# Kernel optimization log

Measured on AMD Instinct MI355X. Metric: run time of the kernel, lower is better.

The kernel has to match this reference:

```python
import jax, jax.numpy as jnp
import numpy as np

NUM_HEADS = 16
DK = 64
DV = 64
MASK_FILL = -10000000000.0


def setup_inputs() -> dict:
    key = jax.random.key(0)
    kq, kk, kv, km = jax.random.split(key, 4)
    B, L, D = 2, 2048, NUM_HEADS * DK
    Q = jax.random.normal(kq, (B, L, D), dtype=jnp.float32)
    K = jax.random.normal(kk, (B, L, D), dtype=jnp.float32)
    V = jax.random.normal(kv, (B, L, NUM_HEADS * DV), dtype=jnp.float32)
    mask = jax.random.randint(km, (B, L, L), 0, 2).astype(jnp.bool_)
    return {"Q": Q, "K": K, "V": V, "mask": mask}


def reference(Q, K, V, mask):
    B, Lq, _ = Q.shape
    Lk = K.shape[1]
    # split heads: [B, H, L, d]
    q = Q.reshape(B, Lq, NUM_HEADS, DK).transpose(0, 2, 1, 3)
    k = K.reshape(B, Lk, NUM_HEADS, DK).transpose(0, 2, 1, 3)
    v = V.reshape(B, Lk, NUM_HEADS, DV).transpose(0, 2, 1, 3)
    # scores [B, H, Lq, Lk]; NOTE: original masks BEFORE scaling by 1/sqrt(dk)
    scores = jnp.einsum("bhqd,bhkd->bhqk", q, k)
    scores = jnp.where(mask[:, None, :, :], MASK_FILL, scores)
    scores = scores / jnp.sqrt(jnp.asarray(DK, dtype=scores.dtype))
    attn = jax.nn.softmax(scores, axis=-1)
    out = jnp.einsum("bhqk,bhkd->bhqd", attn, v)  # [B, H, Lq, dv]
    # concat heads back: [B, Lq, H*dv]
    return out.transpose(0, 2, 1, 3).reshape(B, Lq, NUM_HEADS * DV)
```

## Files before the change

kernel.cpp:

```cpp
#include <hip/hip_runtime.h>
#include <hip/hip_bf16.h>

#define NH 16
#define DH 64
#define LL 2048
#define DM 1024
#define SCALE2 0.1803368801111204f
#define M_STATIC 10.0f
#define THR_C 6.0f
#define NT2 (LL / 128)

typedef __attribute__((ext_vector_type(4))) float f32x4;
typedef __attribute__((ext_vector_type(8))) short bf16x8;
typedef __attribute__((ext_vector_type(4))) short bf16x4;

__device__ __forceinline__ unsigned pk2(float lo, float hi) {
    __hip_bfloat162 h = __float22bfloat162_rn(make_float2(lo, hi));
    union { __hip_bfloat162 h; unsigned u; } c; c.h = h; return c.u;
}
__device__ __forceinline__ bf16x8 cvt8(float4 a, float4 b) {
    union { bf16x8 v; unsigned u[4]; } r;
    r.u[0] = pk2(a.x, a.y); r.u[1] = pk2(a.z, a.w);
    r.u[2] = pk2(b.x, b.y); r.u[3] = pk2(b.z, b.w);
    return r.v;
}
__device__ __forceinline__ float exp2_fast(float x) {
    float y;
    asm("v_exp_f32 %0, %1" : "=v"(y) : "v"(x));
    return y;
}

__global__ __launch_bounds__(256) void pack_mask2(const void* __restrict__ mask,
                                                  unsigned* __restrict__ bits)
{
    const int tid = threadIdx.x;
    const int lane = tid & 63;
    const int* mw = (const int*)mask;
    unsigned long long bad = __ballot((unsigned)mw[lane] > 1u);
    const bool is_int = (bad == 0ULL);

    const int wid = blockIdx.x * 256 + tid;
    const int g = wid & 3;
    const int t = (wid >> 2) & 15;
    const int q64 = wid >> 6;
    unsigned m = 0;
    if (is_int) {
        const int* p = (const int*)mask + (size_t)q64 * LL + t * 128 + 4 * g;
        #pragma unroll
        for (int sub = 0; sub < 2; ++sub)
            #pragma unroll
            for (int ki = 0; ki < 4; ++ki) {
                int4 v = *(const int4*)(p + sub * 64 + ki * 16);
                int base = sub * 16 + ki * 4;
                m |= (v.x ? 1u : 0u) << base;
                m |= (v.y ? 1u : 0u) << (base + 1);
                m |= (v.z ? 1u : 0u) << (base + 2);
                m |= (v.w ? 1u : 0u) << (base + 3);
            }
    } else {
        const unsigned char* pb = (const unsigned char*)mask
                                + (size_t)q64 * LL + t * 128 + 4 * g;
        #pragma unroll
        for (int sub = 0; sub < 2; ++sub)
            #pragma unroll
            for (int ki = 0; ki < 4; ++ki) {
                unsigned v = *(const unsigned*)(pb + sub * 64 + ki * 16);
                int base = sub * 16 + ki * 4;
                m |= (v & 1u) << base;
                m |= ((v >> 8) & 1u) << (base + 1);
                m |= ((v >> 16) & 1u) << (base + 2);
                m |= ((v >> 24) & 1u) << (base + 3);
            }
    }
    bits[wid] = m;
}

__global__ __launch_bounds__(256) void prep_k(const float* __restrict__ K,
                                              short* __restrict__ Kb)
{
    const int kt = blockIdx.x, h = blockIdx.y, b = blockIdx.z;
    const int tid = threadIdx.x;
    const int key = tid >> 2;
    const int c8 = (tid & 3) * 2;
    const float* src = K + ((size_t)b * LL + kt * 64 + key) * DM + h * DH + c8 * 8;
    float4 a = *(const float4*)(src);
    float4 bb = *(const float4*)(src + 4);
    float4 c = *(const float4*)(src + 8);
    float4 d = *(const float4*)(src + 12);
    short* dst = Kb + (((size_t)(b * NH + h) * 32 + kt) << 12);
    *(bf16x8*)&dst[key * 64 + ((c8 ^ (key & 7)) << 3)] = cvt8(a, bb);
    *(bf16x8*)&dst[key * 64 + (((c8 + 1) ^ (key & 7)) << 3)] = cvt8(c, d);
}

__global__ __launch_bounds__(256) void prep_v(const float* __restrict__ V,
                                              short* __restrict__ Vb)
{
    const int kt = blockIdx.x, h = blockIdx.y, b = blockIdx.z;
    const int tid = threadIdx.x;
    const int kp = tid & 31;
    const int dv8 = tid >> 5;
    const float* s0 = V + ((size_t)b * LL + kt * 64 + 2 * kp) * DM + h * DH + dv8 * 8;
    float4 a0 = *(const float4*)(s0);
    float4 a1 = *(const float4*)(s0 + 4);
    float4 b0 = *(const float4*)(s0 + DM);
    float4 b1 = *(const float4*)(s0 + DM + 4);
    float av[8] = {a0.x, a0.y, a0.z, a0.w, a1.x, a1.y, a1.z, a1.w};
    float bv[8] = {b0.x, b0.y, b0.z, b0.w, b1.x, b1.y, b1.z, b1.w};
    short* dst = Vb + (((size_t)(b * NH + h) * 32 + kt) << 12);
    #pragma unroll
    for (int j = 0; j < 8; ++j) {
        int dv = dv8 * 8 + j;
        int off = dv * 64 + (((kp >> 1) ^ (dv & 15)) << 2) + 2 * (kp & 1);
        *(unsigned*)&dst[off] = pk2(av[j], bv[j]);
    }
}

__global__ __launch_bounds__(512, 4) void mha_fwd2(
    const float* __restrict__ Q, const short* __restrict__ Kb,
    const short* __restrict__ Vb, const unsigned* __restrict__ mbits,
    float* __restrict__ out)
{
    const int bid = blockIdx.x;
    const int xcd = bid & 7;
    const int j = bid >> 3;
    const int pair = xcd * 4 + (j >> 4);
    const int qblk = j & 15;
    const int h = pair & 15;
    const int b = pair >> 4;

    const int tid = threadIdx.x;
    const int w = tid >> 6;
    const int lane = tid & 63;
    const int lq = lane & 15;
    const int g = lane >> 4;

    const int qbase = qblk * 128 + w * 16;

    __shared__ short Kt[2][2][4096];
    __shared__ short Vt[2][2][4096];

    const short* Ktile0 = Kb + ((size_t)(b * NH + h) << 17);
    const short* Vtile0 = Vb + ((size_t)(b * NH + h) << 17);
    const unsigned* Mp = mbits + ((size_t)b * LL + qbase + lq) * 64 + g;

    unsigned mnext = Mp[0];
    #pragma unroll
    for (int sub = 0; sub < 2; ++sub) {
        __builtin_amdgcn_global_load_lds(
            (const unsigned*)(Ktile0 + sub * 4096 + w * 512 + lane * 8),
            (unsigned*)&Kt[0][sub][w * 512], 16, 0, 0);
        __builtin_amdgcn_global_load_lds(
            (const unsigned*)(Vtile0 + sub * 4096 + w * 512 + lane * 8),
            (unsigned*)&Vt[0][sub][w * 512], 16, 0, 0);
    }

    bf16x8 qf[2];
    {
        const float* qrow = Q + ((size_t)b * LL + qbase + lq) * DM + h * DH;
        #pragma unroll
        for (int half = 0; half < 2; ++half) {
            const float* src = qrow + half * 32 + g * 8;
            float4 a = *(const float4*)(src);
            float4 c = *(const float4*)(src + 4);
            a.x *= SCALE2; a.y *= SCALE2; a.z *= SCALE2; a.w *= SCALE2;
            c.x *= SCALE2; c.y *= SCALE2; c.z *= SCALE2; c.w *= SCALE2;
            qf[half] = cvt8(a, c);
        }
    }

    f32x4 o[4];
    #pragma unroll
    for (int t = 0; t < 4; ++t) o[t] = (f32x4){0.f, 0.f, 0.f, 0.f};
    f32x4 l_acc = (f32x4){0.f, 0.f, 0.f, 0.f};
    float m_run = M_STATIC;
    const bf16x4 ones = {(short)0x3F80, (short)0x3F80, (short)0x3F80, (short)0x3F80};

    asm volatile("s_waitcnt vmcnt(0)" ::: "memory");
    __builtin_amdgcn_s_barrier();

    #pragma unroll 2
    for (int t = 0; t < NT2; ++t) {
        const int cur = t & 1;
        const unsigned mword = mnext;
        if (t + 1 < NT2) {
            mnext = Mp[(t + 1) * 4];
            const short* kb = Ktile0 + (size_t)(t + 1) * 8192;
            const short* vb = Vtile0 + (size_t)(t + 1) * 8192;
            #pragma unroll
            for (int sub = 0; sub < 2; ++sub) {
                __builtin_amdgcn_global_load_lds(
                    (const unsigned*)(kb + sub * 4096 + w * 512 + lane * 8),
                    (unsigned*)&Kt[cur ^ 1][sub][w * 512], 16, 0, 0);
                __builtin_amdgcn_global_load_lds(
                    (const unsigned*)(vb + sub * 4096 + w * 512 + lane * 8),
                    (unsigned*)&Vt[cur ^ 1][sub][w * 512], 16, 0, 0);
            }
            asm volatile("s_waitcnt vmcnt(5)" ::: "memory");
        } else {
            asm volatile("s_waitcnt vmcnt(0)" ::: "memory");
        }
        __builtin_amdgcn_s_barrier();
        __builtin_amdgcn_sched_barrier(0);

        f32x4 s[8];
        __builtin_amdgcn_s_setprio(1);
        #pragma unroll
        for (int sub = 0; sub < 2; ++sub)
            #pragma unroll
            for (int ki = 0; ki < 4; ++ki) {
                const int row = ki * 16 + lq;
                bf16x8 k0 = *(const bf16x8*)
                    &Kt[cur][sub][row * 64 + ((g ^ (lq & 7)) << 3)];
                bf16x8 k1 = *(const bf16x8*)
                    &Kt[cur][sub][row * 64 + (((4 + g) ^ (lq & 7)) << 3)];
                f32x4 acc = (f32x4){0.f, 0.f, 0.f, 0.f};
                acc = __builtin_amdgcn_mfma_f32_16x16x32_bf16(k0, qf[0], acc, 0, 0, 0);
                acc = __builtin_amdgcn_mfma_f32_16x16x32_bf16(k1, qf[1], acc, 0, 0, 0);
                s[sub * 4 + ki] = acc;
            }
        __builtin_amdgcn_s_setprio(0);

        f32x4 sv[8];
        #pragma unroll
        for (int i = 0; i < 8; ++i) sv[i] = s[i] - m_run;

        f32x4 mx = sv[0];
        #pragma unroll
        for (int i = 1; i < 8; ++i) {
            mx[0] = fmaxf(mx[0], sv[i][0]);
            mx[1] = fmaxf(mx[1], sv[i][1]);
            mx[2] = fmaxf(mx[2], sv[i][2]);
            mx[3] = fmaxf(mx[3], sv[i][3]);
        }
        float pmax = fmaxf(fmaxf(mx[0], mx[1]), fmaxf(mx[2], mx[3]));
        if (!__all(pmax <= THR_C)) {
            float tmax = fmaxf(pmax, __shfl_xor(pmax, 16, 64));
            tmax = fmaxf(tmax, __shfl_xor(tmax, 32, 64));
            float shift = fmaxf(tmax, 0.f);
            float alpha = exp2_fast(-shift);
            m_run += shift;
            #pragma unroll
            for (int q = 0; q < 4; ++q) {
                o[q][0] *= alpha; o[q][1] *= alpha;
                o[q][2] *= alpha; o[q][3] *= alpha;
            }
            l_acc[0] *= alpha; l_acc[1] *= alpha;
            l_acc[2] *= alpha; l_acc[3] *= alpha;
            #pragma unroll
            for (int i = 0; i < 8; ++i) sv[i] = sv[i] - shift;
        }

        float p_[32];
        #pragma unroll
        for (int i = 0; i < 8; ++i)
            #pragma unroll
            for (int r = 0; r < 4; ++r)
                p_[i * 4 + r] = exp2_fast(sv[i][r]);

        const unsigned nword = ~mword;
        #pragma unroll
        for (int idx = 0; idx < 32; ++idx) {
            int keep = (int)(nword << (31 - idx)) >> 31;
            unsigned pu = __builtin_bit_cast(unsigned, p_[idx]) & (unsigned)keep;
            p_[idx] = __builtin_bit_cast(float, pu);
        }

        __builtin_amdgcn_s_setprio(1);
        #pragma unroll
        for (int sub = 0; sub < 2; ++sub)
            #pragma unroll
            for (int ki = 0; ki < 4; ++ki) {
                union { bf16x4 v; unsigned u[2]; } pf;
                pf.u[0] = pk2(p_[sub * 16 + ki * 4 + 0], p_[sub * 16 + ki * 4 + 1]);
                pf.u[1] = pk2(p_[sub * 16 + ki * 4 + 2], p_[sub * 16 + ki * 4 + 3]);
                l_acc = __builtin_amdgcn_mfma_f32_16x16x16bf16_1k(ones, pf.v, l_acc, 0, 0, 0);
                #pragma unroll
                for (int q = 0; q < 4; ++q) {
                    bf16x4 vf = *(const bf16x4*)
                        &Vt[cur][sub][(16 * q + lq) * 64 + (((4 * ki + g) ^ lq) << 2)];
                    o[q] = __builtin_amdgcn_mfma_f32_16x16x16bf16_1k(vf, pf.v, o[q], 0, 0, 0);
                }
            }
        __builtin_amdgcn_s_setprio(0);

        __builtin_amdgcn_sched_barrier(0);
        __builtin_amdgcn_s_barrier();
    }

    float inv = __builtin_amdgcn_rcpf(l_acc[0]);
    float* orow = out + ((size_t)b * LL + qbase + lq) * DM + h * DH;
    #pragma unroll
    for (int t = 0; t < 4; ++t) {
        float4 ov;
        ov.x = o[t][0] * inv; ov.y = o[t][1] * inv;
        ov.z = o[t][2] * inv; ov.w = o[t][3] * inv;
        *(float4*)(orow + 16 * t + 4 * g) = ov;
    }
}

extern "C" void kernel_launch(void* const* d_in, const int* in_sizes, int n_in,
                              void* d_out, int out_size, void* d_ws, size_t ws_size,
                              hipStream_t stream) {
    const float* Q = (const float*)d_in[0];
    const float* K = (const float*)d_in[1];
    const float* V = (const float*)d_in[2];
    const void* mask = d_in[3];
    float* out = (float*)d_out;

    unsigned* bits = (unsigned*)d_ws;
    const size_t MASK_B = (size_t)2 * LL * 64 * 4;
    const size_t KV_B = (size_t)2 * NH * 32 * 4096 * 2;
    short* Kb = (short*)((char*)d_ws + MASK_B);
    short* Vb = (short*)((char*)d_ws + MASK_B + KV_B);

    pack_mask2<<<dim3(2 * LL * 64 / 256), dim3(256), 0, stream>>>(mask, bits);
    prep_k<<<dim3(32, NH, 2), dim3(256), 0, stream>>>(K, Kb);
    prep_v<<<dim3(32, NH, 2), dim3(256), 0, stream>>>(V, Vb);
    mha_fwd2<<<dim3(512), dim3(512), 0, stream>>>(Q, Kb, Vb, bits, out);
}
```

Before: 82.11 us.

## Widen V LDS reads to 128-bit, pre-invert mask bits, relax softmax rescale threshold

Changes the swizzled V tile layout so each lane reads 8 bf16 values with a single 128-bit LDS load that feeds two MFMAs, instead of two 64-bit loads. The mask bits are inverted in the packing kernel so the attention loop no longer negates them. The online-softmax baseline changes from a static offset of 10 with a rescale threshold of 6 to zero with a threshold of 60, and the shift is subtracted only once a rescale has happened. The exp, mask and pack work is interleaved per sub-tile with the PV MFMAs. Raising the threshold lets exp2 arguments grow larger before a rescale, which narrows the headroom before f32 overflow.

Result: no change. 80.69 us (-1.7%).

```diff
diff --git a/kernel.cpp b/kernel.cpp
--- a/kernel.cpp
+++ b/kernel.cpp
@@ -6,8 +6,7 @@
 #define LL 2048
 #define DM 1024
 #define SCALE2 0.1803368801111204f
-#define M_STATIC 10.0f
-#define THR_C 6.0f
+#define GUARD_HI 60.0f
 #define NT2 (LL / 128)
 
 typedef __attribute__((ext_vector_type(4))) float f32x4;
@@ -28,6 +27,11 @@
     float y;
     asm("v_exp_f32 %0, %1" : "=v"(y) : "v"(x));
     return y;
+}
+__device__ __forceinline__ float keepf(float p, unsigned nw, int idx) {
+    int k = (int)(nw << (31 - idx)) >> 31;
+    unsigned pu = __builtin_bit_cast(unsigned, p) & (unsigned)k;
+    return __builtin_bit_cast(float, pu);
 }
 
 __global__ __launch_bounds__(256) void pack_mask2(const void* __restrict__ mask,
@@ -72,7 +76,7 @@
                 m |= ((v >> 24) & 1u) << (base + 3);
             }
     }
-    bits[wid] = m;
+    bits[wid] = ~m;
 }
 
 __global__ __launch_bounds__(256) void prep_k(const float* __restrict__ K,
@@ -107,10 +111,12 @@
     float av[8] = {a0.x, a0.y, a0.z, a0.w, a1.x, a1.y, a1.z, a1.w};
     float bv[8] = {b0.x, b0.y, b0.z, b0.w, b1.x, b1.y, b1.z, b1.w};
     short* dst = Vb + (((size_t)(b * NH + h) * 32 + kt) << 12);
+    const int grp = ((kp >> 4) << 2) | ((kp >> 1) & 3);
+    const int sub4 = (((kp >> 3) & 1) << 2) | ((kp & 1) << 1);
     #pragma unroll
     for (int j = 0; j < 8; ++j) {
         int dv = dv8 * 8 + j;
-        int off = dv * 64 + (((kp >> 1) ^ (dv & 15)) << 2) + 2 * (kp & 1);
+        int off = dv * 64 + ((grp ^ (dv & 7)) << 3) + sub4;
         *(unsigned*)&dst[off] = pk2(av[j], bv[j]);
     }
 }
@@ -172,7 +178,7 @@
     #pragma unroll
     for (int t = 0; t < 4; ++t) o[t] = (f32x4){0.f, 0.f, 0.f, 0.f};
     f32x4 l_acc = (f32x4){0.f, 0.f, 0.f, 0.f};
-    float m_run = M_STATIC;
+    float m_shift = 0.f;
     const bf16x4 ones = {(short)0x3F80, (short)0x3F80, (short)0x3F80, (short)0x3F80};
 
     asm volatile("s_waitcnt vmcnt(0)" ::: "memory");
@@ -181,7 +187,7 @@
     #pragma unroll 2
     for (int t = 0; t < NT2; ++t) {
         const int cur = t & 1;
-        const unsigned mword = mnext;
+        const unsigned nword = mnext;
         if (t + 1 < NT2) {
             mnext = Mp[(t + 1) * 4];
             const short* kb = Ktile0 + (size_t)(t + 1) * 8192;
@@ -202,7 +208,7 @@
         __builtin_amdgcn_s_barrier();
         __builtin_amdgcn_sched_barrier(0);
 
-        f32x4 s[8];
+        f32x4 sAB[2][4];
         __builtin_amdgcn_s_setprio(1);
         #pragma unroll
         for (int sub = 0; sub < 2; ++sub)
@@ -216,29 +222,29 @@
                 f32x4 acc = (f32x4){0.f, 0.f, 0.f, 0.f};
                 acc = __builtin_amdgcn_mfma_f32_16x16x32_bf16(k0, qf[0], acc, 0, 0, 0);
                 acc = __builtin_amdgcn_mfma_f32_16x16x32_bf16(k1, qf[1], acc, 0, 0, 0);
-                s[sub * 4 + ki] = acc;
+                sAB[sub][ki] = acc;
             }
         __builtin_amdgcn_s_setprio(0);
 
-        f32x4 sv[8];
-        #pragma unroll
-        for (int i = 0; i < 8; ++i) sv[i] = s[i] - m_run;
-
-        f32x4 mx = sv[0];
-        #pragma unroll
-        for (int i = 1; i < 8; ++i) {
-            mx[0] = fmaxf(mx[0], sv[i][0]);
-            mx[1] = fmaxf(mx[1], sv[i][1]);
-            mx[2] = fmaxf(mx[2], sv[i][2]);
-            mx[3] = fmaxf(mx[3], sv[i][3]);
-        }
-        float pmax = fmaxf(fmaxf(mx[0], mx[1]), fmaxf(mx[2], mx[3]));
-        if (!__all(pmax <= THR_C)) {
-            float tmax = fmaxf(pmax, __shfl_xor(pmax, 16, 64));
+        float mm[8];
+        #pragma unroll
+        for (int i = 0; i < 8; ++i) {
+            f32x4 v = sAB[i >> 2][i & 3];
+            mm[i] = fmaxf(fmaxf(v[0], v[1]), fmaxf(v[2], v[3]));
+        }
+        float mx = fmaxf(fmaxf(fmaxf(mm[0], mm[1]), fmaxf(mm[2], mm[3])),
+                         fmaxf(fmaxf(mm[4], mm[5]), fmaxf(mm[6], mm[7])));
+        if (__builtin_expect(m_shift != 0.0f, 0)) {
+            #pragma unroll
+            for (int i = 0; i < 8; ++i) sAB[i >> 2][i & 3] = sAB[i >> 2][i & 3] - m_shift;
+            mx -= m_shift;
+        }
+        if (!__all(mx <= GUARD_HI)) {
+            float tmax = fmaxf(mx, __shfl_xor(mx, 16, 64));
             tmax = fmaxf(tmax, __shfl_xor(tmax, 32, 64));
-            float shift = fmaxf(tmax, 0.f);
+            float shift = tmax - 30.0f;
+            m_shift += shift;
             float alpha = exp2_fast(-shift);
-            m_run += shift;
             #pragma unroll
             for (int q = 0; q < 4; ++q) {
                 o[q][0] *= alpha; o[q][1] *= alpha;
@@ -247,41 +253,39 @@
             l_acc[0] *= alpha; l_acc[1] *= alpha;
             l_acc[2] *= alpha; l_acc[3] *= alpha;
             #pragma unroll
-            for (int i = 0; i < 8; ++i) sv[i] = sv[i] - shift;
-        }
-
-        float p_[32];
-        #pragma unroll
-        for (int i = 0; i < 8; ++i)
-            #pragma unroll
-            for (int r = 0; r < 4; ++r)
-                p_[i * 4 + r] = exp2_fast(sv[i][r]);
-
-        const unsigned nword = ~mword;
-        #pragma unroll
-        for (int idx = 0; idx < 32; ++idx) {
-            int keep = (int)(nword << (31 - idx)) >> 31;
-            unsigned pu = __builtin_bit_cast(unsigned, p_[idx]) & (unsigned)keep;
-            p_[idx] = __builtin_bit_cast(float, pu);
-        }
-
-        __builtin_amdgcn_s_setprio(1);
-        #pragma unroll
-        for (int sub = 0; sub < 2; ++sub)
+            for (int i = 0; i < 8; ++i) sAB[i >> 2][i & 3] = sAB[i >> 2][i & 3] - shift;
+        }
+
+        #pragma unroll
+        for (int sub = 0; sub < 2; ++sub) {
+            union { bf16x4 v; unsigned u[2]; } pf[4];
             #pragma unroll
             for (int ki = 0; ki < 4; ++ki) {
-                union { bf16x4 v; unsigned u[2]; } pf;
-                pf.u[0] = pk2(p_[sub * 16 + ki * 4 + 0], p_[sub * 16 + ki * 4 + 1]);
-                pf.u[1] = pk2(p_[sub * 16 + ki * 4 + 2], p_[sub * 16 + ki * 4 + 3]);
-                l_acc = __builtin_amdgcn_mfma_f32_16x16x16bf16_1k(ones, pf.v, l_acc, 0, 0, 0);
+                f32x4 sv = sAB[sub][ki];
+                const int base = sub * 16 + ki * 4;
+                float p0 = keepf(exp2_fast(sv[0]), nword, base + 0);
+                float p1 = keepf(exp2_fast(sv[1]), nword, base + 1);
+                float p2 = keepf(exp2_fast(sv[2]), nword, base + 2);
+                float p3 = keepf(exp2_fast(sv[3]), nword, base + 3);
+                pf[ki].u[0] = pk2(p0, p1);
+                pf[ki].u[1] = pk2(p2, p3);
+                l_acc = __builtin_amdgcn_mfma_f32_16x16x16bf16_1k(ones, pf[ki].v, l_acc, 0, 0, 0);
+            }
+            __builtin_amdgcn_s_setprio(1);
+            #pragma unroll
+            for (int P = 0; P < 2; ++P)
                 #pragma unroll
                 for (int q = 0; q < 4; ++q) {
-                    bf16x4 vf = *(const bf16x4*)
-                        &Vt[cur][sub][(16 * q + lq) * 64 + (((4 * ki + g) ^ lq) << 2)];
-                    o[q] = __builtin_amdgcn_mfma_f32_16x16x16bf16_1k(vf, pf.v, o[q], 0, 0, 0);
+                    const int row = 16 * q + lq;
+                    bf16x8 v8 = *(const bf16x8*)
+                        &Vt[cur][sub][row * 64 + ((((P << 2) + g) ^ (lq & 7)) << 3)];
+                    bf16x4 vlo = {v8[0], v8[1], v8[2], v8[3]};
+                    bf16x4 vhi = {v8[4], v8[5], v8[6], v8[7]};
+                    o[q] = __builtin_amdgcn_mfma_f32_16x16x16bf16_1k(vlo, pf[2 * P].v, o[q], 0, 0, 0);
+                    o[q] = __builtin_amdgcn_mfma_f32_16x16x16bf16_1k(vhi, pf[2 * P + 1].v, o[q], 0, 0, 0);
                 }
-            }
-        __builtin_amdgcn_s_setprio(0);
+            __builtin_amdgcn_s_setprio(0);
+        }
 
         __builtin_amdgcn_sched_barrier(0);
         __builtin_amdgcn_s_barrier();
```
